# Performance work log

Measured on AMD Instinct MI355X. Metric: run time of the kernel, lower is better.

The kernel has to match this reference:

```python
import jax, jax.numpy as jnp
import numpy as np

B, C_FEAT, C_CODE, H, W = 32, 768, 70, 28, 28
FS = 11
NEG = 5
POS_INTRA_SHIFT = 0.18
POS_INTER_SHIFT = 0.12
NEG_INTER_SHIFT = 0.46


def _norm(t):
    # F.normalize(t, dim=1, eps=1e-10)
    n = jnp.sqrt(jnp.sum(t * t, axis=1, keepdims=True))
    return t / jnp.maximum(n, 1e-10)


def _grid_sample(t, coords):
    # torch: F.grid_sample(t, coords.permute(0,2,1,3), padding_mode='border', align_corners=True)
    grid = jnp.transpose(coords, (0, 2, 1, 3))  # [N, Hg, Wg, 2], last dim = (x, y)
    N, C, Hi, Wi = t.shape
    # align_corners=True unnormalize, then border-clip the continuous coordinate
    x = jnp.clip((grid[..., 0] + 1.0) * 0.5 * (Wi - 1), 0.0, Wi - 1.0)
    y = jnp.clip((grid[..., 1] + 1.0) * 0.5 * (Hi - 1), 0.0, Hi - 1.0)
    x0 = jnp.floor(x)
    y0 = jnp.floor(y)
    wx = (x - x0)[:, None]  # broadcast over channel dim
    wy = (y - y0)[:, None]
    x0i = x0.astype(jnp.int32)
    y0i = y0.astype(jnp.int32)
    x1i = jnp.minimum(x0i + 1, Wi - 1)
    y1i = jnp.minimum(y0i + 1, Hi - 1)
    gather = jax.vmap(lambda img, yi, xi: img[:, yi, xi])  # [C,Hg,Wg] per batch elem
    v00 = gather(t, y0i, x0i)
    v01 = gather(t, y0i, x1i)
    v10 = gather(t, y1i, x0i)
    v11 = gather(t, y1i, x1i)
    return (v00 * (1.0 - wx) * (1.0 - wy) + v01 * wx * (1.0 - wy)
            + v10 * (1.0 - wx) * wy + v11 * wx * wy)


def _helper(f1, f2, c1, c2, shift):
    # fd under torch.no_grad -> stop_gradient
    fd = jnp.einsum('nchw,ncij->nhwij', _norm(f1), _norm(f2))
    old_mean = fd.mean()  # pointwise=True branch
    fd = fd - fd.mean(axis=(3, 4), keepdims=True)
    fd = jax.lax.stop_gradient(fd - fd.mean() + old_mean)
    cd = jnp.einsum('nchw,ncij->nhwij', _norm(c1), _norm(c2))
    # zero_clamp=True -> min_val=0.0; stabalize=True -> clamp max 0.8
    loss = -jnp.clip(cd, 0.0, 0.8) * (fd - shift)
    return loss, cd


def _forward(orig_feats, orig_feats_pos, orig_code, orig_code_pos,
             depth_aug_feats, depth_aug_feats_pos, coords1, coords2, perms):
    c1 = coords1 * 2.0 - 1.0
    c2 = coords2 * 2.0 - 1.0
    feats = _grid_sample(orig_feats, c1)
    code = _grid_sample(orig_code, c1)
    feats_pos = _grid_sample(orig_feats_pos, c2)
    code_pos = _grid_sample(orig_code_pos, c2)
    daf = _grid_sample(depth_aug_feats, c1)
    _ = _grid_sample(depth_aug_feats_pos, c2)  # computed (as in torch) but unused

    pos_intra_loss, pos_intra_cd = _helper(daf, daf, code, code, POS_INTRA_SHIFT)
    pos_inter_loss, pos_inter_cd = _helper(feats, feats_pos, code, code_pos, POS_INTER_SHIFT)

    neg_losses, neg_cds = [], []
    for i in range(perms.shape[0]):  # fixed small neg_samples loop
        p = perms[i]
        feats_neg = _grid_sample(orig_feats[p], c2)
        code_neg = _grid_sample(orig_code[p], c2)
        l, cd = _helper(feats, feats_neg, code, code_neg, NEG_INTER_SHIFT)
        neg_losses.append(l)
        neg_cds.append(cd)
    neg_inter_loss = jnp.concatenate(neg_losses, axis=0)
    neg_inter_cd = jnp.concatenate(neg_cds, axis=0)
    return (pos_intra_loss.mean(), pos_intra_cd,
            pos_inter_loss.mean(), pos_inter_cd,
            neg_inter_loss, neg_inter_cd)


def setup_inputs() -> dict:
    key = jax.random.key(0)
    ks = jax.random.split(key, 10)
    rng = np.random.default_rng(0)
    perms = []
    for _ in range(NEG):  # super_perm: derangement-ish permutation
        p = rng.permutation(B)
        p = np.where(p == np.arange(B), p + 1, p) % B
        perms.append(p)
    return {
        'orig_feats': jax.random.normal(ks[0], (B, C_FEAT, H, W), jnp.float32),
        'orig_feats_pos': jax.random.normal(ks[1], (B, C_FEAT, H, W), jnp.float32),
        'orig_salience': jnp.zeros((B, H, W), jnp.float32),
        'orig_salience_pos': jnp.zeros((B, H, W), jnp.float32),
        'orig_code': jax.random.normal(ks[2], (B, C_CODE, H, W), jnp.float32),
        'orig_code_pos': jax.random.normal(ks[3], (B, C_CODE, H, W), jnp.float32),
        'depth_aug_feats': jax.random.normal(ks[4], (B, C_FEAT, H, W), jnp.float32),
        'depth_aug_feats_pos': jax.random.normal(ks[5], (B, C_FEAT, H, W), jnp.float32),
        'coords1': jax.random.uniform(ks[6], (B, FS, FS, 2), jnp.float32),
        'coords2': jax.random.uniform(ks[7], (B, FS, FS, 2), jnp.float32),
        'perms': jnp.asarray(np.stack(perms), dtype=jnp.int32),
    }


def reference(orig_feats, orig_feats_pos, orig_salience, orig_salience_pos,
              orig_code, orig_code_pos, depth_aug_feats, depth_aug_feats_pos,
              coords1, coords2, perms):
    # use_salience=False: salience tensors unused
    return _forward(orig_feats, orig_feats_pos, orig_code, orig_code_pos,
                    depth_aug_feats, depth_aug_feats_pos, coords1, coords2, perms)
```

## Files before the change

### kernel.cpp

```cpp
#include <hip/hip_runtime.h>

#define CF 768
#define CCODE 70
#define NPIX 784
#define P 121
#define NB 32
#define NTOTF 468512.0f

#define OFF_PI_SCALAR 0
#define OFF_PI_CD 1
#define OFF_PO_SCALAR 468513
#define OFF_PO_CD 468514
#define OFF_NEG_LOSS 937026
#define OFF_NEG_CD 3279586

#define WS_BSUMS 0
#define WS_ADDT 768
#define WS_INVF 1024
#define WS_INVC 33792
#define WS_FRAG_FLOAT 62464
#define FEAT_FRAG_SHORTS 98304
#define CODE_FRAG_SHORTS 12288
#define FEATS_TOTAL_SHORTS (8 * 32 * FEAT_FRAG_SHORTS)
#define CODE_BASE_SHORTS FEATS_TOTAL_SHORTS
#define CODE_TOTAL_SHORTS (7 * 32 * CODE_FRAG_SHORTS)
#define WS_NEED2 (WS_FRAG_FLOAT + (FEATS_TOTAL_SHORTS + CODE_TOTAL_SHORTS) / 2)

typedef __attribute__((ext_vector_type(8))) short short8;
typedef __attribute__((ext_vector_type(4))) float f32x4;
typedef unsigned short ushort_t;
typedef unsigned int uint_t;

__device__ __forceinline__ float samp4(const float* __restrict__ img, int c,
                                       const int4 o, const float4 w) {
  const float* p = img + c * NPIX;
  return w.x * p[o.x] + w.y * p[o.y] + w.z * p[o.z] + w.w * p[o.w];
}

__device__ __forceinline__ void mkcoord(const float* cp, int4* o, float4* w) {
  float x = fminf(fmaxf(cp[0] * 27.f, 0.f), 27.f);
  float y = fminf(fmaxf(cp[1] * 27.f, 0.f), 27.f);
  float x0f = floorf(x), y0f = floorf(y);
  int x0 = (int)x0f, y0 = (int)y0f;
  int x1 = min(x0 + 1, 27), y1 = min(y0 + 1, 27);
  float wx = x - x0f, wy = y - y0f;
  *o = make_int4(y0 * 28 + x0, y0 * 28 + x1, y1 * 28 + x0, y1 * 28 + x1);
  *w = make_float4((1.f - wx) * (1.f - wy), wx * (1.f - wy),
                   (1.f - wx) * wy, wx * wy);
}

__device__ __forceinline__ void mkcoord2(const float* cp, int2* o, float4* w) {
  float x = fminf(fmaxf(cp[0] * 27.f, 0.f), 27.f);
  float y = fminf(fmaxf(cp[1] * 27.f, 0.f), 27.f);
  float x0f = floorf(x), y0f = floorf(y);
  int x0 = (int)x0f, y0 = (int)y0f;
  int y1 = min(y0 + 1, 27);
  float wx = x - x0f, wy = y - y0f;
  bool sh = (x0 >= 27);
  int xb = sh ? 26 : x0;
  float wa0 = sh ? 0.f : (1.f - wx) * (1.f - wy);
  float wa1 = sh ? (1.f - wy) : wx * (1.f - wy);
  float wb0 = sh ? 0.f : (1.f - wx) * wy;
  float wb1 = sh ? wy : wx * wy;
  *o = make_int2(y0 * 28 + xb, y1 * 28 + xb);
  *w = make_float4(wa0, wa1, wb0, wb1);
}

__device__ __forceinline__ ushort_t f2bf(float x) {
  uint_t u = __float_as_uint(x);
  u += 0x7fffu + ((u >> 16) & 1u);
  return (ushort_t)(u >> 16);
}

__device__ __forceinline__ float bflo(uint_t u) {
  return __uint_as_float(u << 16);
}
__device__ __forceinline__ float bfhi(uint_t u) {
  return __uint_as_float(u & 0xffff0000u);
}

__global__ __launch_bounds__(256) void presample_hoist(
    const float* __restrict__ OF, const float* __restrict__ OFP,
    const float* __restrict__ OC, const float* __restrict__ OCP,
    const float* __restrict__ DAF,
    const float* __restrict__ CO1, const float* __restrict__ CO2,
    const int* __restrict__ PERMS, float* __restrict__ ws) {
  ushort_t* frags = (ushort_t*)(ws + WS_FRAG_FLOAT);
  __shared__ float planes[8 * NPIX];
  __shared__ int sh_slot[16], sh_n[16], sh_cb[16];
  __shared__ int sh_ncs;
  const int job = (int)(((long long)blockIdx.x * 405) % 1216);
  const int tid = threadIdx.x;

  int tensor, m, g0, G;
  if (job < 384) { tensor = 0; m = job / 12; g0 = (job - m * 12) * 8; G = 8; }
  else if (job < 768) { int j = job - 384; tensor = 1; m = j / 12; g0 = (j - m * 12) * 8; G = 8; }
  else if (job < 1152) { int j = job - 768; tensor = 2; m = j / 12; g0 = (j - m * 12) * 8; G = 8; }
  else if (job < 1184) { tensor = 3; m = job - 1152; g0 = 0; G = 12; }
  else { tensor = 4; m = job - 1184; g0 = 0; G = 12; }

  const float* src;
  int nch;
  bool feat;
  if (tensor == 0) { src = OF + (size_t)m * CF * NPIX; nch = CF; feat = true; }
  else if (tensor == 1) { src = DAF + (size_t)m * CF * NPIX; nch = CF; feat = true; }
  else if (tensor == 2) { src = OFP + (size_t)m * CF * NPIX; nch = CF; feat = true; }
  else if (tensor == 3) { src = OC + (size_t)m * CCODE * NPIX; nch = CCODE; feat = false; }
  else { src = OCP + (size_t)m * CCODE * NPIX; nch = CCODE; feat = false; }

  if (tid == 0) {
    int cnt = 0;
    if (tensor == 0) {
      sh_slot[0] = 1; sh_n[0] = m; sh_cb[0] = 0; cnt = 1;
      for (int i = 0; i < 5; ++i)
        for (int k = 0; k < NB; ++k)
          if (PERMS[i * NB + k] == m) {
            sh_slot[cnt] = 3 + i; sh_n[cnt] = k; sh_cb[cnt] = 1; ++cnt;
          }
    } else if (tensor == 1) { sh_slot[0] = 0; sh_n[0] = m; sh_cb[0] = 0; cnt = 1; }
    else if (tensor == 2) { sh_slot[0] = 2; sh_n[0] = m; sh_cb[0] = 1; cnt = 1; }
    else if (tensor == 3) {
      sh_slot[0] = 0; sh_n[0] = m; sh_cb[0] = 0; cnt = 1;
      for (int i = 0; i < 5; ++i)
        for (int k = 0; k < NB; ++k)
          if (PERMS[i * NB + k] == m) {
            sh_slot[cnt] = 2 + i; sh_n[cnt] = k; sh_cb[cnt] = 1; ++cnt;
          }
    } else { sh_slot[0] = 1; sh_n[0] = m; sh_cb[0] = 1; cnt = 1; }
    sh_ncs = cnt;
  }

  float4 buf0, buf1, buf2, buf3, buf4, buf5, buf6;
#define LOAD_OCT(OCT)                                                        \
  {                                                                          \
    const int c0_ = (OCT) * 8;                                               \
    int valid_ = nch - c0_;                                                  \
    valid_ = valid_ > 8 ? 8 : (valid_ < 0 ? 0 : valid_);                     \
    const int lim4_ = valid_ * (NPIX / 4);                                   \
    const float4* sc_ = (const float4*)(src + (size_t)c0_ * NPIX);           \
    int e_;                                                                  \
    e_ = tid;          buf0 = (e_ < lim4_) ? sc_[e_] : make_float4(0,0,0,0); \
    e_ = tid + 256;    buf1 = (e_ < lim4_) ? sc_[e_] : make_float4(0,0,0,0); \
    e_ = tid + 512;    buf2 = (e_ < lim4_) ? sc_[e_] : make_float4(0,0,0,0); \
    e_ = tid + 768;    buf3 = (e_ < lim4_) ? sc_[e_] : make_float4(0,0,0,0); \
    e_ = tid + 1024;   buf4 = (e_ < lim4_) ? sc_[e_] : make_float4(0,0,0,0); \
    e_ = tid + 1280;   buf5 = (e_ < lim4_) ? sc_[e_] : make_float4(0,0,0,0); \
    e_ = tid + 1536;                                                         \
    buf6 = (e_ < 1568 && e_ < lim4_) ? sc_[e_] : make_float4(0,0,0,0);       \
  }

  LOAD_OCT(g0);
  __syncthreads();

  const int total = sh_ncs * 128;
  int2 o_0, o_1, o_2, o_3, o_4, o_5;
  float4 w_0, w_1, w_2, w_3, w_4, w_5;
  uint_t b_0 = 0, b_1 = 0, b_2 = 0, b_3 = 0, b_4 = 0, b_5 = 0;
#define SETUP_SLOT(J, OV, WV, BV)                                            \
  {                                                                          \
    const int s_ = tid + (J) * 256;                                          \
    OV = make_int2(0, 0);                                                    \
    WV = make_float4(0.f, 0.f, 0.f, 0.f);                                    \
    if (s_ < total) {                                                        \
      const int cs_ = s_ >> 7, pt_ = s_ & 127;                               \
      const int slot_ = sh_slot[cs_], n_ = sh_n[cs_];                        \
      const float* cb_ = sh_cb[cs_] ? CO2 : CO1;                             \
      size_t fb_ = feat ? (size_t)(slot_ * 32 + n_) * FEAT_FRAG_SHORTS       \
                        : CODE_BASE_SHORTS +                                 \
                              (size_t)(slot_ * 32 + n_) * CODE_FRAG_SHORTS;  \
      BV = (uint_t)(fb_ + ((size_t)((pt_ >> 4) * 64 + (pt_ & 15)) << 3));    \
      if (pt_ < P) {                                                         \
        int gi_ = pt_ / 11, gj_ = pt_ - gi_ * 11;                            \
        mkcoord2(cb_ + (((n_ * 11 + gj_) * 11 + gi_) << 1), &OV, &WV);       \
      }                                                                      \
    }                                                                        \
  }
  SETUP_SLOT(0, o_0, w_0, b_0)
  SETUP_SLOT(1, o_1, w_1, b_1)
  SETUP_SLOT(2, o_2, w_2, b_2)
  SETUP_SLOT(3, o_3, w_3, b_3)
  SETUP_SLOT(4, o_4, w_4, b_4)
  SETUP_SLOT(5, o_5, w_5, b_5)
#undef SETUP_SLOT

#define DO_SLOT(J, OV, WV, BV)                                               \
  if (tid + (J) * 256 < total) {                                             \
    float v_[8];                                                             \
    _Pragma("unroll") for (int i_ = 0; i_ < 8; ++i_) {                       \
      const float* pl_ = planes + i_ * NPIX;                                 \
      v_[i_] = WV.x * pl_[OV.x] + WV.y * pl_[OV.x + 1] +                     \
               WV.z * pl_[OV.y] + WV.w * pl_[OV.y + 1];                      \
    }                                                                        \
    uint4 q_;                                                                \
    q_.x = (uint_t)f2bf(v_[0]) | ((uint_t)f2bf(v_[1]) << 16);                \
    q_.y = (uint_t)f2bf(v_[2]) | ((uint_t)f2bf(v_[3]) << 16);                \
    q_.z = (uint_t)f2bf(v_[4]) | ((uint_t)f2bf(v_[5]) << 16);                \
    q_.w = (uint_t)f2bf(v_[6]) | ((uint_t)f2bf(v_[7]) << 16);                \
    *(uint4*)(frags + BV + octoff) = q_;                                     \
  }

  for (int g = 0; g < G; ++g) {
    const int o = g0 + g;
    if (g) __syncthreads();
    {
      float4* pl4 = (float4*)planes;
      int e;
      e = tid;        pl4[e] = buf0;
      e = tid + 256;  pl4[e] = buf1;
      e = tid + 512;  pl4[e] = buf2;
      e = tid + 768;  pl4[e] = buf3;
      e = tid + 1024; pl4[e] = buf4;
      e = tid + 1280; pl4[e] = buf5;
      e = tid + 1536; if (e < 1568) pl4[e] = buf6;
    }
    __syncthreads();
    if (g + 1 < G) LOAD_OCT(g0 + g + 1);

    const uint_t octoff = (uint_t)((o >> 2) * 4096 + (o & 3) * 128);
    DO_SLOT(0, o_0, w_0, b_0)
    DO_SLOT(1, o_1, w_1, b_1)
    DO_SLOT(2, o_2, w_2, b_2)
    DO_SLOT(3, o_3, w_3, b_3)
    DO_SLOT(4, o_4, w_4, b_4)
    DO_SLOT(5, o_5, w_5, b_5)
  }
#undef DO_SLOT
#undef LOAD_OCT
}

__global__ __launch_bounds__(128) void norms_kernel(float* __restrict__ ws) {
  const ushort_t* frags = (const ushort_t*)(ws + WS_FRAG_FLOAT);
  const int b = blockIdx.x, p = threadIdx.x;
  float s = 0.f;
  if (b < 256) {
    const int slot = b >> 5, n = b & 31;
    const uint4* F = (const uint4*)(frags + (size_t)(slot * 32 + n) * FEAT_FRAG_SHORTS);
    for (int kp = 0; kp < 24; ++kp) {
#pragma unroll
      for (int lg = 0; lg < 4; ++lg) {
        uint4 q = F[(kp * 8 + (p >> 4)) * 64 + lg * 16 + (p & 15)];
        float a;
        a = bflo(q.x); s = fmaf(a, a, s); a = bfhi(q.x); s = fmaf(a, a, s);
        a = bflo(q.y); s = fmaf(a, a, s); a = bfhi(q.y); s = fmaf(a, a, s);
        a = bflo(q.z); s = fmaf(a, a, s); a = bfhi(q.z); s = fmaf(a, a, s);
        a = bflo(q.w); s = fmaf(a, a, s); a = bfhi(q.w); s = fmaf(a, a, s);
      }
    }
    ws[WS_INVF + (slot * 32 + n) * 128 + p] = 1.f / fmaxf(sqrtf(s), 1e-10f);
  } else {
    const int b2 = b - 256;
    const int slot = b2 >> 5, n = b2 & 31;
    const uint4* F = (const uint4*)(frags + CODE_BASE_SHORTS +
                                    (size_t)(slot * 32 + n) * CODE_FRAG_SHORTS);
#pragma unroll
    for (int kp = 0; kp < 3; ++kp) {
#pragma unroll
      for (int lg = 0; lg < 4; ++lg) {
        uint4 q = F[(kp * 8 + (p >> 4)) * 64 + lg * 16 + (p & 15)];
        float a;
        a = bflo(q.x); s = fmaf(a, a, s); a = bfhi(q.x); s = fmaf(a, a, s);
        a = bflo(q.y); s = fmaf(a, a, s); a = bfhi(q.y); s = fmaf(a, a, s);
        a = bflo(q.z); s = fmaf(a, a, s); a = bfhi(q.z); s = fmaf(a, a, s);
        a = bflo(q.w); s = fmaf(a, a, s); a = bfhi(q.w); s = fmaf(a, a, s);
      }
    }
    ws[WS_INVC + (slot * 32 + n) * 128 + p] = 1.f / fmaxf(sqrtf(s), 1e-10f);
  }
}

__global__ __launch_bounds__(256) void gram_mfma(float* __restrict__ ws,
                                                 float* __restrict__ out) {
  const ushort_t* frags = (const ushort_t*)(ws + WS_FRAG_FLOAT);
  const int bid = blockIdx.x, pair = bid >> 5, n = bid & 31;
  const int tid = threadIdx.x, wave = tid >> 6, lane = tid & 63;
  __shared__ float invAf[128], invBf[128], invAc[128], invBc[128];
  __shared__ float red[4][3];
  const int afslot = (pair == 0) ? 0 : 1;
  const int bfslot = (pair == 0) ? 0 : (pair == 1 ? 2 : 3 + (pair - 2));
  const int bcslot = (pair == 0) ? 0 : (pair == 1 ? 1 : 2 + (pair - 2));
  if (tid < 128) {
    invAf[tid] = ws[WS_INVF + (afslot * 32 + n) * 128 + tid];
    invBf[tid] = ws[WS_INVF + (bfslot * 32 + n) * 128 + tid];
    invAc[tid] = ws[WS_INVC + (0 * 32 + n) * 128 + tid];
    invBc[tid] = ws[WS_INVC + (bcslot * 32 + n) * 128 + tid];
  }
  __syncthreads();

  const short8* Af = (const short8*)(frags + (size_t)(afslot * 32 + n) * FEAT_FRAG_SHORTS);
  const short8* Bf = (const short8*)(frags + (size_t)(bfslot * 32 + n) * FEAT_FRAG_SHORTS);

  f32x4 acc[2][8];
#pragma unroll
  for (int j = 0; j < 2; ++j)
#pragma unroll
    for (int t = 0; t < 8; ++t) acc[j][t] = (f32x4){0.f, 0.f, 0.f, 0.f};

#pragma unroll 2
  for (int kp = 0; kp < 24; ++kp) {
    short8 a0 = Af[(kp * 8 + 2 * wave) * 64 + lane];
    short8 a1 = Af[(kp * 8 + 2 * wave + 1) * 64 + lane];
    short8 bv[8];
#pragma unroll
    for (int t = 0; t < 8; ++t) bv[t] = Bf[(kp * 8 + t) * 64 + lane];
#pragma unroll
    for (int t = 0; t < 8; ++t) {
      acc[0][t] = __builtin_amdgcn_mfma_f32_16x16x32_bf16(a0, bv[t], acc[0][t], 0, 0, 0);
      acc[1][t] = __builtin_amdgcn_mfma_f32_16x16x32_bf16(a1, bv[t], acc[1][t], 0, 0, 0);
    }
  }

  const int lane4 = (lane >> 4) << 2;
  const int cl15 = lane & 15;
  float sfd = 0.f;
#pragma unroll
  for (int j = 0; j < 2; ++j) {
    const int rb = (2 * wave + j) * 16 + lane4;
    const float ivr0 = invAf[rb], ivr1 = invAf[rb + 1], ivr2 = invAf[rb + 2],
                ivr3 = invAf[rb + 3];
    float rs0 = 0.f, rs1 = 0.f, rs2 = 0.f, rs3 = 0.f;
#pragma unroll
    for (int t = 0; t < 8; ++t) {
      const float ivc = invBf[t * 16 + cl15];
      float v0 = acc[j][t].x * ivr0 * ivc;
      float v1 = acc[j][t].y * ivr1 * ivc;
      float v2 = acc[j][t].z * ivr2 * ivc;
      float v3 = acc[j][t].w * ivr3 * ivc;
      acc[j][t].x = v0; acc[j][t].y = v1; acc[j][t].z = v2; acc[j][t].w = v3;
      rs0 += v0; rs1 += v1; rs2 += v2; rs3 += v3;
    }
    sfd += rs0 + rs1 + rs2 + rs3;
    rs0 += __shfl_xor(rs0, 1); rs0 += __shfl_xor(rs0, 2);
    rs0 += __shfl_xor(rs0, 4); rs0 += __shfl_xor(rs0, 8);
    rs1 += __shfl_xor(rs1, 1); rs1 += __shfl_xor(rs1, 2);
    rs1 += __shfl_xor(rs1, 4); rs1 += __shfl_xor(rs1, 8);
    rs2 += __shfl_xor(rs2, 1); rs2 += __shfl_xor(rs2, 2);
    rs2 += __shfl_xor(rs2, 4); rs2 += __shfl_xor(rs2, 8);
    rs3 += __shfl_xor(rs3, 1); rs3 += __shfl_xor(rs3, 2);
    rs3 += __shfl_xor(rs3, 4); rs3 += __shfl_xor(rs3, 8);
    const float rm0 = rs0 * (1.f / 121.f), rm1 = rs1 * (1.f / 121.f);
    const float rm2 = rs2 * (1.f / 121.f), rm3 = rs3 * (1.f / 121.f);
#pragma unroll
    for (int t = 0; t < 8; ++t) {
      acc[j][t].x -= rm0; acc[j][t].y -= rm1; acc[j][t].z -= rm2; acc[j][t].w -= rm3;
    }
  }

  int cd_base, loss_base = 0;
  if (pair == 0) cd_base = OFF_PI_CD + n * 14641;
  else if (pair == 1) cd_base = OFF_PO_CD + n * 14641;
  else {
    int t0 = ((pair - 2) * NB + n) * 14641;
    cd_base = OFF_NEG_CD + t0;
    loss_base = OFF_NEG_LOSS + t0;
  }

  if (pair >= 2) {
#pragma unroll
    for (int j = 0; j < 2; ++j) {
      const int rb = (2 * wave + j) * 16 + lane4;
      if (rb < P) {
#pragma unroll
        for (int t = 0; t < 8; ++t) {
          const int c = t * 16 + cl15;
          if (c < P) {
            float* o = out + loss_base + rb * P + c;
            o[0] = acc[j][t].x;
            if (rb + 1 < P) o[P] = acc[j][t].y;
            if (rb + 2 < P) o[2 * P] = acc[j][t].z;
            if (rb + 3 < P) o[3 * P] = acc[j][t].w;
          }
        }
      }
    }
  }

  const short8* Ac = (const short8*)(frags + CODE_BASE_SHORTS + (size_t)n * CODE_FRAG_SHORTS);
  const short8* Bc = (const short8*)(frags + CODE_BASE_SHORTS + (size_t)(bcslot * 32 + n) * CODE_FRAG_SHORTS);
  f32x4 cacc[2][8];
#pragma unroll
  for (int j = 0; j < 2; ++j)
#pragma unroll
    for (int t = 0; t < 8; ++t) cacc[j][t] = (f32x4){0.f, 0.f, 0.f, 0.f};
#pragma unroll
  for (int kp = 0; kp < 3; ++kp) {
    short8 a0 = Ac[(kp * 8 + 2 * wave) * 64 + lane];
    short8 a1 = Ac[(kp * 8 + 2 * wave + 1) * 64 + lane];
    short8 bv[8];
#pragma unroll
    for (int t = 0; t < 8; ++t) bv[t] = Bc[(kp * 8 + t) * 64 + lane];
#pragma unroll
    for (int t = 0; t < 8; ++t) {
      cacc[0][t] = __builtin_amdgcn_mfma_f32_16x16x32_bf16(a0, bv[t], cacc[0][t], 0, 0, 0);
      cacc[1][t] = __builtin_amdgcn_mfma_f32_16x16x32_bf16(a1, bv[t], cacc[1][t], 0, 0, 0);
    }
  }

  float s1 = 0.f, s2 = 0.f;
#pragma unroll
  for (int j = 0; j < 2; ++j) {
    const int rb = (2 * wave + j) * 16 + lane4;
    const float ivr0 = invAc[rb], ivr1 = invAc[rb + 1], ivr2 = invAc[rb + 2],
                ivr3 = invAc[rb + 3];
#pragma unroll
    for (int t = 0; t < 8; ++t) {
      const int c = t * 16 + cl15;
      const float ivc = invBc[c];
      float c0v = cacc[j][t].x * ivr0 * ivc;
      float c1v = cacc[j][t].y * ivr1 * ivc;
      float c2v = cacc[j][t].z * ivr2 * ivc;
      float c3v = cacc[j][t].w * ivr3 * ivc;
      if (c < P && rb < P) {
        float* o = out + cd_base + rb * P + c;
        o[0] = c0v;
        if (rb + 1 < P) o[P] = c1v;
        if (rb + 2 < P) o[2 * P] = c2v;
        if (rb + 3 < P) o[3 * P] = c3v;
      }
      if (pair < 2) {
        float cl0 = fminf(fmaxf(c0v, 0.f), 0.8f);
        float cl1 = fminf(fmaxf(c1v, 0.f), 0.8f);
        float cl2 = fminf(fmaxf(c2v, 0.f), 0.8f);
        float cl3 = fminf(fmaxf(c3v, 0.f), 0.8f);
        s1 = fmaf(cl0, acc[j][t].x, s1);
        s1 = fmaf(cl1, acc[j][t].y, s1);
        s1 = fmaf(cl2, acc[j][t].z, s1);
        s1 = fmaf(cl3, acc[j][t].w, s1);
        s2 += cl0 + cl1 + cl2 + cl3;
      }
    }
  }

#pragma unroll
  for (int m = 1; m < 64; m <<= 1) {
    sfd += __shfl_xor(sfd, m);
    s1 += __shfl_xor(s1, m);
    s2 += __shfl_xor(s2, m);
  }
  if ((tid & 63) == 0) { red[wave][0] = sfd; red[wave][1] = s1; red[wave][2] = s2; }
  __syncthreads();
  if (tid == 0) {
    float a = 0.f, b2 = 0.f, c2 = 0.f;
    for (int w = 0; w < 4; ++w) { a += red[w][0]; b2 += red[w][1]; c2 += red[w][2]; }
    float* bsums = ws + WS_BSUMS;
    bsums[bid * 3 + 0] = a;
    bsums[bid * 3 + 1] = b2;
    bsums[bid * 3 + 2] = c2;
  }
}

__global__ void loss_finish2(float* __restrict__ ws, float* __restrict__ out) {
  __shared__ float s[7][3];
  const float* bsums = ws + WS_BSUMS;
  float* addterm = ws + WS_ADDT;
  int tid = threadIdx.x;
  if (tid < 21) {
    int pr = tid / 3, k = tid % 3;
    float a = 0.f;
    for (int i = 0; i < 32; ++i) a += bsums[(pr * 32 + i) * 3 + k];
    s[pr][k] = a;
  }
  __syncthreads();
  if (tid == 0) {
    const float invN = 1.f / NTOTF;
    out[OFF_PI_SCALAR] = -(s[0][1] + (s[0][0] * invN - 0.18f) * s[0][2]) * invN;
    out[OFF_PO_SCALAR] = -(s[1][1] + (s[1][0] * invN - 0.12f) * s[1][2]) * invN;
  }
  if (tid >= 1 && tid < 6) addterm[tid - 1] = s[tid + 1][0] / NTOTF - 0.46f;
}

__global__ __launch_bounds__(256) void neg_loss_kernel(
    float* __restrict__ lossr, const float* __restrict__ cdr,
    const float* __restrict__ addterm) {
  __shared__ float at[5];
  if (threadIdx.x < 5) at[threadIdx.x] = addterm[threadIdx.x];
  __syncthreads();
  const int total4 = 5 * 117128;
  float4* l4 = (float4*)lossr;
  const float4* c4 = (const float4*)cdr;
  for (int e = blockIdx.x * 256 + threadIdx.x; e < total4; e += gridDim.x * 256) {
    int k = e / 117128;
    float4 cd = c4[e];
    float4 fv = l4[e];
    float a = at[k];
    float4 r;
    r.x = -fminf(fmaxf(cd.x, 0.f), 0.8f) * (fv.x + a);
    r.y = -fminf(fmaxf(cd.y, 0.f), 0.8f) * (fv.y + a);
    r.z = -fminf(fmaxf(cd.z, 0.f), 0.8f) * (fv.z + a);
    r.w = -fminf(fmaxf(cd.w, 0.f), 0.8f) * (fv.w + a);
    l4[e] = r;
  }
}


__global__ __launch_bounds__(256) void loss_main_fb(
    const float* __restrict__ OF, const float* __restrict__ OFP,
    const float* __restrict__ OC, const float* __restrict__ OCP,
    const float* __restrict__ DAF,
    const float* __restrict__ CO1, const float* __restrict__ CO2,
    const int* __restrict__ PERMS,
    float* __restrict__ out, float* __restrict__ bsums) {
  const int b = blockIdx.x;
  const int pair = b >> 7;
  const int rem = b & 127;
  const int n = rem >> 2;
  const int rg = rem & 3;
  const int row_start = rg * 31;
  const int rcount = min(31, P - row_start);
  const int tid = threadIdx.x;
  const int tx = tid & 15, ty = tid >> 4;

  const float *F1, *F2, *C1, *C2, *CB;
  if (pair == 0) {
    F1 = DAF + (size_t)n * CF * NPIX; F2 = F1;
    C1 = OC + (size_t)n * CCODE * NPIX; C2 = C1;
    CB = CO1;
  } else if (pair == 1) {
    F1 = OF + (size_t)n * CF * NPIX; F2 = OFP + (size_t)n * CF * NPIX;
    C1 = OC + (size_t)n * CCODE * NPIX; C2 = OCP + (size_t)n * CCODE * NPIX;
    CB = CO2;
  } else {
    int n2 = PERMS[(pair - 2) * NB + n];
    F1 = OF + (size_t)n * CF * NPIX; F2 = OF + (size_t)n2 * CF * NPIX;
    C1 = OC + (size_t)n * CCODE * NPIX; C2 = OC + (size_t)n2 * CCODE * NPIX;
    CB = CO2;
  }

  __shared__ int4 Bo[P];
  __shared__ float4 Bw[P];
  __shared__ int4 Ao[32];
  __shared__ float4 Aw[32];
  __shared__ float Abuf[CCODE][32];
  __shared__ float Bbuf[CCODE][128];
  __shared__ float invA[32], invB[128];
  __shared__ float red[4][3];

  if (tid < P) {
    int gi = tid / 11, gj = tid - gi * 11;
    const float* cp = CB + (((n * 11 + gj) * 11 + gi) << 1);
    mkcoord(cp, &Bo[tid], &Bw[tid]);
  } else if (tid >= 128 && tid < 160) {
    int r = tid - 128;
    int q = row_start + r;
    if (q < P) {
      int gi = q / 11, gj = q - gi * 11;
      const float* cp = CO1 + (((n * 11 + gj) * 11 + gi) << 1);
      mkcoord(cp, &Ao[r], &Aw[r]);
    }
  }
  __syncthreads();

  float acc[2][2][4];
#pragma unroll
  for (int kr = 0; kr < 2; ++kr)
#pragma unroll
    for (int m = 0; m < 2; ++m)
#pragma unroll
      for (int u = 0; u < 4; ++u) acc[kr][m][u] = 0.f;
  float ansq = 0.f, bnsq = 0.f;

  for (int ch = 0; ch < 12; ++ch) {
    const int c0 = ch * 64;
    if (ch) __syncthreads();
    for (int e = tid; e < 64 * 128; e += 256) {
      int col = e & 127, cc = e >> 7;
      float v = 0.f;
      if (col < P) v = samp4(F2, c0 + cc, Bo[col], Bw[col]);
      Bbuf[cc][col] = v;
    }
    for (int e = tid; e < 64 * 32; e += 256) {
      int col = e & 31, cc = e >> 5;
      float v = 0.f;
      if (col < rcount) v = samp4(F1, c0 + cc, Ao[col], Aw[col]);
      Abuf[cc][col] = v;
    }
    __syncthreads();
    if (tid < 128) {
      float s = 0.f;
      for (int cc = 0; cc < 64; ++cc) { float v = Bbuf[cc][tid]; s = fmaf(v, v, s); }
      bnsq += s;
    } else if (tid < 160) {
      int r = tid - 128;
      float s = 0.f;
      for (int cc = 0; cc < 64; ++cc) { float v = Abuf[cc][r]; s = fmaf(v, v, s); }
      ansq += s;
    }
    for (int cc = 0; cc < 64; ++cc) {
      const float2 av = *(const float2*)&Abuf[cc][ty * 2];
      const float4 b0 = *(const float4*)&Bbuf[cc][tx * 4];
      const float4 b1 = *(const float4*)&Bbuf[cc][tx * 4 + 64];
      float a[2] = {av.x, av.y};
      float bb[2][4] = {{b0.x, b0.y, b0.z, b0.w}, {b1.x, b1.y, b1.z, b1.w}};
#pragma unroll
      for (int kr = 0; kr < 2; ++kr)
#pragma unroll
        for (int m = 0; m < 2; ++m)
#pragma unroll
          for (int u = 0; u < 4; ++u)
            acc[kr][m][u] = fmaf(a[kr], bb[m][u], acc[kr][m][u]);
    }
  }
  __syncthreads();
  if (tid < 128) invB[tid] = (tid < P) ? 1.f / fmaxf(sqrtf(bnsq), 1e-10f) : 0.f;
  else if (tid < 160) {
    int r = tid - 128;
    invA[r] = (r < rcount) ? 1.f / fmaxf(sqrtf(ansq), 1e-10f) : 0.f;
  }
  __syncthreads();

  float ia[2] = {invA[2 * ty], invA[2 * ty + 1]};
  float ib[2][4];
#pragma unroll
  for (int m = 0; m < 2; ++m)
#pragma unroll
    for (int u = 0; u < 4; ++u) ib[m][u] = invB[m * 64 + tx * 4 + u];

  float fdc[2][2][4];
  float sfd = 0.f;
#pragma unroll
  for (int kr = 0; kr < 2; ++kr) {
    float part = 0.f;
#pragma unroll
    for (int m = 0; m < 2; ++m)
#pragma unroll
      for (int u = 0; u < 4; ++u) {
        float v = acc[kr][m][u] * ia[kr] * ib[m][u];
        fdc[kr][m][u] = v;
        part += v;
      }
    sfd += part;
    float rs = part;
#pragma unroll
    for (int s = 1; s < 16; s <<= 1) rs += __shfl_xor(rs, s, 16);
    float rowm = rs * (1.f / 121.f);
#pragma unroll
    for (int m = 0; m < 2; ++m)
#pragma unroll
      for (int u = 0; u < 4; ++u) fdc[kr][m][u] -= rowm;
  }
  __syncthreads();

  for (int e = tid; e < CCODE * 128; e += 256) {
    int col = e & 127, cc = e >> 7;
    float v = 0.f;
    if (col < P) v = samp4(C2, cc, Bo[col], Bw[col]);
    Bbuf[cc][col] = v;
  }
  for (int e = tid; e < CCODE * 32; e += 256) {
    int col = e & 31, cc = e >> 5;
    float v = 0.f;
    if (col < rcount) v = samp4(C1, cc, Ao[col], Aw[col]);
    Abuf[cc][col] = v;
  }
  __syncthreads();
  if (tid < 128) {
    float s = 0.f;
    for (int cc = 0; cc < CCODE; ++cc) { float v = Bbuf[cc][tid]; s = fmaf(v, v, s); }
    invB[tid] = (tid < P) ? 1.f / fmaxf(sqrtf(s), 1e-10f) : 0.f;
  } else if (tid < 160) {
    int r = tid - 128;
    float s = 0.f;
    for (int cc = 0; cc < CCODE; ++cc) { float v = Abuf[cc][r]; s = fmaf(v, v, s); }
    invA[r] = (r < rcount) ? 1.f / fmaxf(sqrtf(s), 1e-10f) : 0.f;
  }
  float cacc[2][2][4];
#pragma unroll
  for (int kr = 0; kr < 2; ++kr)
#pragma unroll
    for (int m = 0; m < 2; ++m)
#pragma unroll
      for (int u = 0; u < 4; ++u) cacc[kr][m][u] = 0.f;
  for (int cc = 0; cc < CCODE; ++cc) {
    const float2 av = *(const float2*)&Abuf[cc][ty * 2];
    const float4 b0 = *(const float4*)&Bbuf[cc][tx * 4];
    const float4 b1 = *(const float4*)&Bbuf[cc][tx * 4 + 64];
    float a[2] = {av.x, av.y};
    float bb[2][4] = {{b0.x, b0.y, b0.z, b0.w}, {b1.x, b1.y, b1.z, b1.w}};
#pragma unroll
    for (int kr = 0; kr < 2; ++kr)
#pragma unroll
      for (int m = 0; m < 2; ++m)
#pragma unroll
        for (int u = 0; u < 4; ++u)
          cacc[kr][m][u] = fmaf(a[kr], bb[m][u], cacc[kr][m][u]);
  }
  __syncthreads();
  float iac[2] = {invA[2 * ty], invA[2 * ty + 1]};
  float ibc[2][4];
#pragma unroll
  for (int m = 0; m < 2; ++m)
#pragma unroll
    for (int u = 0; u < 4; ++u) ibc[m][u] = invB[m * 64 + tx * 4 + u];

  int cd_base, loss_base = 0;
  if (pair == 0) cd_base = OFF_PI_CD + n * 14641;
  else if (pair == 1) cd_base = OFF_PO_CD + n * 14641;
  else {
    int t = ((pair - 2) * NB + n) * 14641;
    cd_base = OFF_NEG_CD + t;
    loss_base = OFF_NEG_LOSS + t;
  }

  float s1 = 0.f, s2 = 0.f;
#pragma unroll
  for (int kr = 0; kr < 2; ++kr) {
    int r = 2 * ty + kr;
    if (r < rcount) {
      int rglob = row_start + r;
#pragma unroll
      for (int m = 0; m < 2; ++m)
#pragma unroll
        for (int u = 0; u < 4; ++u) {
          int c = m * 64 + tx * 4 + u;
          if (c < P) {
            float cdv = cacc[kr][m][u] * iac[kr] * ibc[m][u];
            int idx = rglob * P + c;
            out[cd_base + idx] = cdv;
            float cl = fminf(fmaxf(cdv, 0.f), 0.8f);
            float fv = fdc[kr][m][u];
            if (pair < 2) { s1 = fmaf(cl, fv, s1); s2 += cl; }
            else out[loss_base + idx] = fv;
          }
        }
    }
  }

#pragma unroll
  for (int s = 1; s < 64; s <<= 1) {
    sfd += __shfl_xor(sfd, s);
    s1 += __shfl_xor(s1, s);
    s2 += __shfl_xor(s2, s);
  }
  int wv = tid >> 6;
  if ((tid & 63) == 0) { red[wv][0] = sfd; red[wv][1] = s1; red[wv][2] = s2; }
  __syncthreads();
  if (tid == 0) {
    float a = 0.f, bb = 0.f, cc = 0.f;
    for (int w = 0; w < 4; ++w) { a += red[w][0]; bb += red[w][1]; cc += red[w][2]; }
    bsums[b * 3 + 0] = a;
    bsums[b * 3 + 1] = bb;
    bsums[b * 3 + 2] = cc;
  }
}

__global__ void loss_finish_fb(const float* __restrict__ bsums,
                               float* __restrict__ out,
                               float* __restrict__ addterm) {
  __shared__ float s[7][3];
  int tid = threadIdx.x;
  if (tid < 21) {
    int pr = tid / 3, k = tid % 3;
    float a = 0.f;
    const float* p = bsums + (pr * 128) * 3 + k;
    for (int i = 0; i < 128; ++i) a += p[i * 3];
    s[pr][k] = a;
  }
  __syncthreads();
  if (tid == 0) {
    const float invN = 1.f / NTOTF;
    out[OFF_PI_SCALAR] = -(s[0][1] + (s[0][0] * invN - 0.18f) * s[0][2]) * invN;
    out[OFF_PO_SCALAR] = -(s[1][1] + (s[1][0] * invN - 0.12f) * s[1][2]) * invN;
  }
  if (tid >= 1 && tid < 6) addterm[tid - 1] = s[tid + 1][0] / NTOTF - 0.46f;
}

__global__ __launch_bounds__(256) void neg_loss_fb(
    float* __restrict__ lossr, const float* __restrict__ cdr,
    const float* __restrict__ addterm) {
  __shared__ float at[5];
  if (threadIdx.x < 5) at[threadIdx.x] = addterm[threadIdx.x];
  __syncthreads();
  const int total = 5 * 468512;
  for (int e = blockIdx.x * 256 + threadIdx.x; e < total; e += gridDim.x * 256) {
    int k = e / 468512;
    float cdv = cdr[e];
    float cl = fminf(fmaxf(cdv, 0.f), 0.8f);
    lossr[e] = -cl * (lossr[e] + at[k]);
  }
}

extern "C" void kernel_launch(void* const* d_in, const int* in_sizes, int n_in,
                              void* d_out, int out_size, void* d_ws,
                              size_t ws_size, hipStream_t stream) {
  const float* OF = (const float*)d_in[0];
  const float* OFP = (const float*)d_in[1];
  const float* OC = (const float*)d_in[4];
  const float* OCP = (const float*)d_in[5];
  const float* DAF = (const float*)d_in[6];
  const float* CO1 = (const float*)d_in[8];
  const float* CO2 = (const float*)d_in[9];
  const int* PERMS = (const int*)d_in[10];
  float* out = (float*)d_out;
  float* ws = (float*)d_ws;

  if (ws_size >= (size_t)WS_NEED2 * sizeof(float)) {
    hipLaunchKernelGGL(presample_hoist, dim3(1216), dim3(256), 0, stream,
                       OF, OFP, OC, OCP, DAF, CO1, CO2, PERMS, ws);
    hipLaunchKernelGGL(norms_kernel, dim3(480), dim3(128), 0, stream, ws);
    hipLaunchKernelGGL(gram_mfma, dim3(224), dim3(256), 0, stream, ws, out);
    hipLaunchKernelGGL(loss_finish2, dim3(1), dim3(64), 0, stream, ws, out);
    hipLaunchKernelGGL(neg_loss_kernel, dim3(1024), dim3(256), 0, stream,
                       out + OFF_NEG_LOSS, out + OFF_NEG_CD, ws + WS_ADDT);
  } else {
    float* bsums = ws;
    float* addterm = bsums + 896 * 3;
    hipLaunchKernelGGL(loss_main_fb, dim3(896), dim3(256), 0, stream,
                       OF, OFP, OC, OCP, DAF, CO1, CO2, PERMS, out, bsums);
    hipLaunchKernelGGL(loss_finish_fb, dim3(1), dim3(64), 0, stream,
                       bsums, out, addterm);
    hipLaunchKernelGGL(neg_loss_fb, dim3(2048), dim3(256), 0, stream,
                       out + OFF_NEG_LOSS, out + OFF_NEG_CD, addterm);
  }
}
```

Measured before the change: 145.2 us.

## Fuse norm computation into presample and split gram blocks in half

```diff
diff --git a/kernel.cpp b/kernel.cpp
--- a/kernel.cpp
+++ b/kernel.cpp
@@ -15,10 +15,10 @@
 #define OFF_NEG_CD 3279586
 
 #define WS_BSUMS 0
-#define WS_ADDT 768
-#define WS_INVF 1024
-#define WS_INVC 33792
-#define WS_FRAG_FLOAT 62464
+#define WS_ADDT 1536
+#define WS_NSQF 2048
+#define WS_NSQC 395264
+#define WS_FRAG_FLOAT 423936
 #define FEAT_FRAG_SHORTS 98304
 #define CODE_FRAG_SHORTS 12288
 #define FEATS_TOTAL_SHORTS (8 * 32 * FEAT_FRAG_SHORTS)
@@ -72,14 +72,7 @@
   return (ushort_t)(u >> 16);
 }
 
-__device__ __forceinline__ float bflo(uint_t u) {
-  return __uint_as_float(u << 16);
-}
-__device__ __forceinline__ float bfhi(uint_t u) {
-  return __uint_as_float(u & 0xffff0000u);
-}
-
-__global__ __launch_bounds__(256) void presample_hoist(
+__global__ __launch_bounds__(256) void presample_fz(
     const float* __restrict__ OF, const float* __restrict__ OFP,
     const float* __restrict__ OC, const float* __restrict__ OCP,
     const float* __restrict__ DAF,
@@ -153,10 +146,13 @@
   __syncthreads();
 
   const int total = sh_ncs * 128;
+  const int sub = g0 >> 3;
   int2 o_0, o_1, o_2, o_3, o_4, o_5;
   float4 w_0, w_1, w_2, w_3, w_4, w_5;
   uint_t b_0 = 0, b_1 = 0, b_2 = 0, b_3 = 0, b_4 = 0, b_5 = 0;
-#define SETUP_SLOT(J, OV, WV, BV)                                            \
+  uint_t nq_0 = 0, nq_1 = 0, nq_2 = 0, nq_3 = 0, nq_4 = 0, nq_5 = 0;
+  float sq_0 = 0.f, sq_1 = 0.f, sq_2 = 0.f, sq_3 = 0.f, sq_4 = 0.f, sq_5 = 0.f;
+#define SETUP_SLOT(J, OV, WV, BV, NQV)                                       \
   {                                                                          \
     const int s_ = tid + (J) * 256;                                          \
     OV = make_int2(0, 0);                                                    \
@@ -169,27 +165,31 @@
                         : CODE_BASE_SHORTS +                                 \
                               (size_t)(slot_ * 32 + n_) * CODE_FRAG_SHORTS;  \
       BV = (uint_t)(fb_ + ((size_t)((pt_ >> 4) * 64 + (pt_ & 15)) << 3));    \
+      NQV = feat ? (uint_t)(WS_NSQF +                                        \
+                            ((slot_ * 32 + n_) * 12 + sub) * 128 + pt_)      \
+                 : (uint_t)(WS_NSQC + (slot_ * 32 + n_) * 128 + pt_);        \
       if (pt_ < P) {                                                         \
         int gi_ = pt_ / 11, gj_ = pt_ - gi_ * 11;                            \
         mkcoord2(cb_ + (((n_ * 11 + gj_) * 11 + gi_) << 1), &OV, &WV);       \
       }                                                                      \
     }                                                                        \
   }
-  SETUP_SLOT(0, o_0, w_0, b_0)
-  SETUP_SLOT(1, o_1, w_1, b_1)
-  SETUP_SLOT(2, o_2, w_2, b_2)
-  SETUP_SLOT(3, o_3, w_3, b_3)
-  SETUP_SLOT(4, o_4, w_4, b_4)
-  SETUP_SLOT(5, o_5, w_5, b_5)
+  SETUP_SLOT(0, o_0, w_0, b_0, nq_0)
+  SETUP_SLOT(1, o_1, w_1, b_1, nq_1)
+  SETUP_SLOT(2, o_2, w_2, b_2, nq_2)
+  SETUP_SLOT(3, o_3, w_3, b_3, nq_3)
+  SETUP_SLOT(4, o_4, w_4, b_4, nq_4)
+  SETUP_SLOT(5, o_5, w_5, b_5, nq_5)
 #undef SETUP_SLOT
 
-#define DO_SLOT(J, OV, WV, BV)                                               \
+#define DO_SLOT(J, OV, WV, BV, SQV)                                          \
   if (tid + (J) * 256 < total) {                                             \
     float v_[8];                                                             \
     _Pragma("unroll") for (int i_ = 0; i_ < 8; ++i_) {                       \
       const float* pl_ = planes + i_ * NPIX;                                 \
       v_[i_] = WV.x * pl_[OV.x] + WV.y * pl_[OV.x + 1] +                     \
                WV.z * pl_[OV.y] + WV.w * pl_[OV.y + 1];                      \
+      SQV = fmaf(v_[i_], v_[i_], SQV);                                       \
     }                                                                        \
     uint4 q_;                                                                \
     q_.x = (uint_t)f2bf(v_[0]) | ((uint_t)f2bf(v_[1]) << 16);                \
@@ -217,61 +217,30 @@
     if (g + 1 < G) LOAD_OCT(g0 + g + 1);
 
     const uint_t octoff = (uint_t)((o >> 2) * 4096 + (o & 3) * 128);
-    DO_SLOT(0, o_0, w_0, b_0)
-    DO_SLOT(1, o_1, w_1, b_1)
-    DO_SLOT(2, o_2, w_2, b_2)
-    DO_SLOT(3, o_3, w_3, b_3)
-    DO_SLOT(4, o_4, w_4, b_4)
-    DO_SLOT(5, o_5, w_5, b_5)
+    DO_SLOT(0, o_0, w_0, b_0, sq_0)
+    DO_SLOT(1, o_1, w_1, b_1, sq_1)
+    DO_SLOT(2, o_2, w_2, b_2, sq_2)
+    DO_SLOT(3, o_3, w_3, b_3, sq_3)
+    DO_SLOT(4, o_4, w_4, b_4, sq_4)
+    DO_SLOT(5, o_5, w_5, b_5, sq_5)
   }
 #undef DO_SLOT
 #undef LOAD_OCT
-}
-
-__global__ __launch_bounds__(128) void norms_kernel(float* __restrict__ ws) {
+
+  if (tid < total) ws[nq_0] = sq_0;
+  if (tid + 256 < total) ws[nq_1] = sq_1;
+  if (tid + 512 < total) ws[nq_2] = sq_2;
+  if (tid + 768 < total) ws[nq_3] = sq_3;
+  if (tid + 1024 < total) ws[nq_4] = sq_4;
+  if (tid + 1280 < total) ws[nq_5] = sq_5;
+}
+
+__global__ __launch_bounds__(256) void gram_mfma2(float* __restrict__ ws,
+                                                  float* __restrict__ out) {
   const ushort_t* frags = (const ushort_t*)(ws + WS_FRAG_FLOAT);
-  const int b = blockIdx.x, p = threadIdx.x;
-  float s = 0.f;
-  if (b < 256) {
-    const int slot = b >> 5, n = b & 31;
-    const uint4* F = (const uint4*)(frags + (size_t)(slot * 32 + n) * FEAT_FRAG_SHORTS);
-    for (int kp = 0; kp < 24; ++kp) {
-#pragma unroll
-      for (int lg = 0; lg < 4; ++lg) {
-        uint4 q = F[(kp * 8 + (p >> 4)) * 64 + lg * 16 + (p & 15)];
-        float a;
-        a = bflo(q.x); s = fmaf(a, a, s); a = bfhi(q.x); s = fmaf(a, a, s);
-        a = bflo(q.y); s = fmaf(a, a, s); a = bfhi(q.y); s = fmaf(a, a, s);
-        a = bflo(q.z); s = fmaf(a, a, s); a = bfhi(q.z); s = fmaf(a, a, s);
-        a = bflo(q.w); s = fmaf(a, a, s); a = bfhi(q.w); s = fmaf(a, a, s);
-      }
-    }
-    ws[WS_INVF + (slot * 32 + n) * 128 + p] = 1.f / fmaxf(sqrtf(s), 1e-10f);
-  } else {
-    const int b2 = b - 256;
-    const int slot = b2 >> 5, n = b2 & 31;
-    const uint4* F = (const uint4*)(frags + CODE_BASE_SHORTS +
-                                    (size_t)(slot * 32 + n) * CODE_FRAG_SHORTS);
-#pragma unroll
-    for (int kp = 0; kp < 3; ++kp) {
-#pragma unroll
-      for (int lg = 0; lg < 4; ++lg) {
-        uint4 q = F[(kp * 8 + (p >> 4)) * 64 + lg * 16 + (p & 15)];
-        float a;
-        a = bflo(q.x); s = fmaf(a, a, s); a = bfhi(q.x); s = fmaf(a, a, s);
-        a = bflo(q.y); s = fmaf(a, a, s); a = bfhi(q.y); s = fmaf(a, a, s);
-        a = bflo(q.z); s = fmaf(a, a, s); a = bfhi(q.z); s = fmaf(a, a, s);
-        a = bflo(q.w); s = fmaf(a, a, s); a = bfhi(q.w); s = fmaf(a, a, s);
-      }
-    }
-    ws[WS_INVC + (slot * 32 + n) * 128 + p] = 1.f / fmaxf(sqrtf(s), 1e-10f);
-  }
-}
-
-__global__ __launch_bounds__(256) void gram_mfma(float* __restrict__ ws,
-                                                 float* __restrict__ out) {
-  const ushort_t* frags = (const ushort_t*)(ws + WS_FRAG_FLOAT);
-  const int bid = blockIdx.x, pair = bid >> 5, n = bid & 31;
+  const int bid = blockIdx.x;
+  const int half = bid & 1, pairn = bid >> 1;
+  const int pair = pairn >> 5, n = pairn & 31;
   const int tid = threadIdx.x, wave = tid >> 6, lane = tid & 63;
   __shared__ float invAf[128], invBf[128], invAc[128], invBc[128];
   __shared__ float red[4][3];
@@ -279,56 +248,61 @@
   const int bfslot = (pair == 0) ? 0 : (pair == 1 ? 2 : 3 + (pair - 2));
   const int bcslot = (pair == 0) ? 0 : (pair == 1 ? 1 : 2 + (pair - 2));
   if (tid < 128) {
-    invAf[tid] = ws[WS_INVF + (afslot * 32 + n) * 128 + tid];
-    invBf[tid] = ws[WS_INVF + (bfslot * 32 + n) * 128 + tid];
-    invAc[tid] = ws[WS_INVC + (0 * 32 + n) * 128 + tid];
-    invBc[tid] = ws[WS_INVC + (bcslot * 32 + n) * 128 + tid];
+    float s;
+    const float* p;
+    p = ws + WS_NSQF + (size_t)(afslot * 32 + n) * 12 * 128 + tid;
+    s = 0.f;
+#pragma unroll
+    for (int u = 0; u < 12; ++u) s += p[u * 128];
+    invAf[tid] = 1.f / fmaxf(sqrtf(s), 1e-10f);
+    p = ws + WS_NSQF + (size_t)(bfslot * 32 + n) * 12 * 128 + tid;
+    s = 0.f;
+#pragma unroll
+    for (int u = 0; u < 12; ++u) s += p[u * 128];
+    invBf[tid] = 1.f / fmaxf(sqrtf(s), 1e-10f);
+    invAc[tid] = 1.f / fmaxf(sqrtf(ws[WS_NSQC + (0 * 32 + n) * 128 + tid]), 1e-10f);
+    invBc[tid] = 1.f / fmaxf(sqrtf(ws[WS_NSQC + (bcslot * 32 + n) * 128 + tid]), 1e-10f);
   }
   __syncthreads();
 
   const short8* Af = (const short8*)(frags + (size_t)(afslot * 32 + n) * FEAT_FRAG_SHORTS);
   const short8* Bf = (const short8*)(frags + (size_t)(bfslot * 32 + n) * FEAT_FRAG_SHORTS);
-
-  f32x4 acc[2][8];
-#pragma unroll
-  for (int j = 0; j < 2; ++j)
-#pragma unroll
-    for (int t = 0; t < 8; ++t) acc[j][t] = (f32x4){0.f, 0.f, 0.f, 0.f};
+  const int rt = half * 4 + wave;
+
+  f32x4 acc[8];
+#pragma unroll
+  for (int t = 0; t < 8; ++t) acc[t] = (f32x4){0.f, 0.f, 0.f, 0.f};
 
 #pragma unroll 2
   for (int kp = 0; kp < 24; ++kp) {
-    short8 a0 = Af[(kp * 8 + 2 * wave) * 64 + lane];
-    short8 a1 = Af[(kp * 8 + 2 * wave + 1) * 64 + lane];
+    short8 a0 = Af[(kp * 8 + rt) * 64 + lane];
     short8 bv[8];
 #pragma unroll
     for (int t = 0; t < 8; ++t) bv[t] = Bf[(kp * 8 + t) * 64 + lane];
 #pragma unroll
-    for (int t = 0; t < 8; ++t) {
-      acc[0][t] = __builtin_amdgcn_mfma_f32_16x16x32_bf16(a0, bv[t], acc[0][t], 0, 0, 0);
-      acc[1][t] = __builtin_amdgcn_mfma_f32_16x16x32_bf16(a1, bv[t], acc[1][t], 0, 0, 0);
-    }
+    for (int t = 0; t < 8; ++t)
+      acc[t] = __builtin_amdgcn_mfma_f32_16x16x32_bf16(a0, bv[t], acc[t], 0, 0, 0);
   }
 
   const int lane4 = (lane >> 4) << 2;
   const int cl15 = lane & 15;
+  const int rb = rt * 16 + lane4;
   float sfd = 0.f;
-#pragma unroll
-  for (int j = 0; j < 2; ++j) {
-    const int rb = (2 * wave + j) * 16 + lane4;
+  {
     const float ivr0 = invAf[rb], ivr1 = invAf[rb + 1], ivr2 = invAf[rb + 2],
                 ivr3 = invAf[rb + 3];
     float rs0 = 0.f, rs1 = 0.f, rs2 = 0.f, rs3 = 0.f;
 #pragma unroll
     for (int t = 0; t < 8; ++t) {
       const float ivc = invBf[t * 16 + cl15];
-      float v0 = acc[j][t].x * ivr0 * ivc;
-      float v1 = acc[j][t].y * ivr1 * ivc;
-      float v2 = acc[j][t].z * ivr2 * ivc;
-      float v3 = acc[j][t].w * ivr3 * ivc;
-      acc[j][t].x = v0; acc[j][t].y = v1; acc[j][t].z = v2; acc[j][t].w = v3;
+      float v0 = acc[t].x * ivr0 * ivc;
+      float v1 = acc[t].y * ivr1 * ivc;
+      float v2 = acc[t].z * ivr2 * ivc;
+      float v3 = acc[t].w * ivr3 * ivc;
+      acc[t].x = v0; acc[t].y = v1; acc[t].z = v2; acc[t].w = v3;
       rs0 += v0; rs1 += v1; rs2 += v2; rs3 += v3;
     }
-    sfd += rs0 + rs1 + rs2 + rs3;
+    sfd = rs0 + rs1 + rs2 + rs3;
     rs0 += __shfl_xor(rs0, 1); rs0 += __shfl_xor(rs0, 2);
     rs0 += __shfl_xor(rs0, 4); rs0 += __shfl_xor(rs0, 8);
     rs1 += __shfl_xor(rs1, 1); rs1 += __shfl_xor(rs1, 2);
@@ -341,7 +315,7 @@
     const float rm2 = rs2 * (1.f / 121.f), rm3 = rs3 * (1.f / 121.f);
 #pragma unroll
     for (int t = 0; t < 8; ++t) {
-      acc[j][t].x -= rm0; acc[j][t].y -= rm1; acc[j][t].z -= rm2; acc[j][t].w -= rm3;
+      acc[t].x -= rm0; acc[t].y -= rm1; acc[t].z -= rm2; acc[t].w -= rm3;
     }
   }
 
@@ -354,61 +328,48 @@
     loss_base = OFF_NEG_LOSS + t0;
   }
 
-  if (pair >= 2) {
-#pragma unroll
-    for (int j = 0; j < 2; ++j) {
-      const int rb = (2 * wave + j) * 16 + lane4;
-      if (rb < P) {
-#pragma unroll
-        for (int t = 0; t < 8; ++t) {
-          const int c = t * 16 + cl15;
-          if (c < P) {
-            float* o = out + loss_base + rb * P + c;
-            o[0] = acc[j][t].x;
-            if (rb + 1 < P) o[P] = acc[j][t].y;
-            if (rb + 2 < P) o[2 * P] = acc[j][t].z;
-            if (rb + 3 < P) o[3 * P] = acc[j][t].w;
-          }
-        }
+  if (pair >= 2 && rb < P) {
+#pragma unroll
+    for (int t = 0; t < 8; ++t) {
+      const int c = t * 16 + cl15;
+      if (c < P) {
+        float* o = out + loss_base + rb * P + c;
+        o[0] = acc[t].x;
+        if (rb + 1 < P) o[P] = acc[t].y;
+        if (rb + 2 < P) o[2 * P] = acc[t].z;
+        if (rb + 3 < P) o[3 * P] = acc[t].w;
       }
     }
   }
 
   const short8* Ac = (const short8*)(frags + CODE_BASE_SHORTS + (size_t)n * CODE_FRAG_SHORTS);
   const short8* Bc = (const short8*)(frags + CODE_BASE_SHORTS + (size_t)(bcslot * 32 + n) * CODE_FRAG_SHORTS);
-  f32x4 cacc[2][8];
-#pragma unroll
-  for (int j = 0; j < 2; ++j)
-#pragma unroll
-    for (int t = 0; t < 8; ++t) cacc[j][t] = (f32x4){0.f, 0.f, 0.f, 0.f};
+  f32x4 cacc[8];
+#pragma unroll
+  for (int t = 0; t < 8; ++t) cacc[t] = (f32x4){0.f, 0.f, 0.f, 0.f};
 #pragma unroll
   for (int kp = 0; kp < 3; ++kp) {
-    short8 a0 = Ac[(kp * 8 + 2 * wave) * 64 + lane];
-    short8 a1 = Ac[(kp * 8 + 2 * wave + 1) * 64 + lane];
+    short8 a0 = Ac[(kp * 8 + rt) * 64 + lane];
     short8 bv[8];
 #pragma unroll
     for (int t = 0; t < 8; ++t) bv[t] = Bc[(kp * 8 + t) * 64 + lane];
 #pragma unroll
-    for (int t = 0; t < 8; ++t) {
-      cacc[0][t] = __builtin_amdgcn_mfma_f32_16x16x32_bf16(a0, bv[t], cacc[0][t], 0, 0, 0);
-      cacc[1][t] = __builtin_amdgcn_mfma_f32_16x16x32_bf16(a1, bv[t], cacc[1][t], 0, 0, 0);
-    }
+    for (int t = 0; t < 8; ++t)
+      cacc[t] = __builtin_amdgcn_mfma_f32_16x16x32_bf16(a0, bv[t], cacc[t], 0, 0, 0);
   }
 
   float s1 = 0.f, s2 = 0.f;
-#pragma unroll
-  for (int j = 0; j < 2; ++j) {
-    const int rb = (2 * wave + j) * 16 + lane4;
+  {
     const float ivr0 = invAc[rb], ivr1 = invAc[rb + 1], ivr2 = invAc[rb + 2],
                 ivr3 = invAc[rb + 3];
 #pragma unroll
     for (int t = 0; t < 8; ++t) {
       const int c = t * 16 + cl15;
       const float ivc = invBc[c];
-      float c0v = cacc[j][t].x * ivr0 * ivc;
-      float c1v = cacc[j][t].y * ivr1 * ivc;
-      float c2v = cacc[j][t].z * ivr2 * ivc;
-      float c3v = cacc[j][t].w * ivr3 * ivc;
+      float c0v = cacc[t].x * ivr0 * ivc;
+      float c1v = cacc[t].y * ivr1 * ivc;
+      float c2v = cacc[t].z * ivr2 * ivc;
+      float c3v = cacc[t].w * ivr3 * ivc;
       if (c < P && rb < P) {
         float* o = out + cd_base + rb * P + c;
         o[0] = c0v;
@@ -421,10 +382,10 @@
         float cl1 = fminf(fmaxf(c1v, 0.f), 0.8f);
         float cl2 = fminf(fmaxf(c2v, 0.f), 0.8f);
         float cl3 = fminf(fmaxf(c3v, 0.f), 0.8f);
-        s1 = fmaf(cl0, acc[j][t].x, s1);
-        s1 = fmaf(cl1, acc[j][t].y, s1);
-        s1 = fmaf(cl2, acc[j][t].z, s1);
-        s1 = fmaf(cl3, acc[j][t].w, s1);
+        s1 = fmaf(cl0, acc[t].x, s1);
+        s1 = fmaf(cl1, acc[t].y, s1);
+        s1 = fmaf(cl2, acc[t].z, s1);
+        s1 = fmaf(cl3, acc[t].w, s1);
         s2 += cl0 + cl1 + cl2 + cl3;
       }
     }
@@ -448,7 +409,7 @@
   }
 }
 
-__global__ void loss_finish2(float* __restrict__ ws, float* __restrict__ out) {
+__global__ void loss_finish3(float* __restrict__ ws, float* __restrict__ out) {
   __shared__ float s[7][3];
   const float* bsums = ws + WS_BSUMS;
   float* addterm = ws + WS_ADDT;
@@ -456,7 +417,7 @@
   if (tid < 21) {
     int pr = tid / 3, k = tid % 3;
     float a = 0.f;
-    for (int i = 0; i < 32; ++i) a += bsums[(pr * 32 + i) * 3 + k];
+    for (int i = 0; i < 64; ++i) a += bsums[(pr * 64 + i) * 3 + k];
     s[pr][k] = a;
   }
   __syncthreads();
@@ -793,12 +754,11 @@
   float* ws = (float*)d_ws;
 
   if (ws_size >= (size_t)WS_NEED2 * sizeof(float)) {
-    hipLaunchKernelGGL(presample_hoist, dim3(1216), dim3(256), 0, stream,
+    hipLaunchKernelGGL(presample_fz, dim3(1216), dim3(256), 0, stream,
                        OF, OFP, OC, OCP, DAF, CO1, CO2, PERMS, ws);
-    hipLaunchKernelGGL(norms_kernel, dim3(480), dim3(128), 0, stream, ws);
-    hipLaunchKernelGGL(gram_mfma, dim3(224), dim3(256), 0, stream, ws, out);
-    hipLaunchKernelGGL(loss_finish2, dim3(1), dim3(64), 0, stream, ws, out);
-    hipLaunchKernelGGL(neg_loss_kernel, dim3(1024), dim3(256), 0, stream,
+    hipLaunchKernelGGL(gram_mfma2, dim3(448), dim3(256), 0, stream, ws, out);
+    hipLaunchKernelGGL(loss_finish3, dim3(1), dim3(64), 0, stream, ws, out);
+    hipLaunchKernelGGL(neg_loss_kernel, dim3(2048), dim3(256), 0, stream,
                        out + OFF_NEG_LOSS, out + OFF_NEG_CD, ws + WS_ADDT);
   } else {
     float* bsums = ws;
```

Result: faster. 139.7 us (-3.8%).
